# Performance work log

Hardware: AMD Instinct MI355X
Metric: run time of the kernel (lower is better)

The kernel has to match this reference:

```python
import jax, jax.numpy as jnp
import numpy as np

# Gemma2-9B layer config
HID = 3584
H = 16          # query heads
KV = 8          # kv heads
G = H // KV     # GQA group size
DH = 256        # head dim
INTER = 14336
WINDOW = 1024   # sliding window size
LOGIT_CAP = 50.0
SCALING = 256.0 ** -0.5   # query_pre_attn_scalar ** -0.5
EPS = 1e-6
ROPE_BASE = 10000.0
B, S = 2, 2048


def gemma_rmsnorm(x, w, eps=EPS):
    # Gemma RMSNorm: fp32 compute, scale by (1 + w)
    xf = x.astype(jnp.float32)
    var = jnp.mean(xf * xf, axis=-1, keepdims=True)
    return (xf * jax.lax.rsqrt(var + eps) * (1.0 + w.astype(jnp.float32))).astype(x.dtype)


def apply_rope(pos, x):
    # neox-style rotary embedding; x: [B, S, n_heads, DH], pos: [B, S]
    half = DH // 2
    inv_freq = 1.0 / (ROPE_BASE ** (jnp.arange(0, half, dtype=jnp.float32) / half * 1.0))
    inv_freq = 1.0 / (ROPE_BASE ** (jnp.arange(0, DH, 2, dtype=jnp.float32) / DH))
    ang = pos.astype(jnp.float32)[..., None] * inv_freq          # [B, S, half]
    cos = jnp.cos(ang)[:, :, None, :]                            # [B, S, 1, half]
    sin = jnp.sin(ang)[:, :, None, :]
    x1, x2 = x[..., :half], x[..., half:]
    return jnp.concatenate([x1 * cos - x2 * sin, x2 * cos + x1 * sin], axis=-1).astype(x.dtype)


def setup_inputs() -> dict:
    key = jax.random.key(0)
    ks = jax.random.split(key, 12)
    s = 0.02
    inp = {
        "hidden_states": jax.random.normal(ks[0], (B, S, HID), dtype=jnp.float32),
        "positions": jnp.tile(jnp.arange(S, dtype=jnp.int32)[None, :], (B, 1)),
        "in_ln_w": jax.random.normal(ks[1], (HID,), dtype=jnp.float32) * s,
        "post_attn_ln_w": jax.random.normal(ks[2], (HID,), dtype=jnp.float32) * s,
        "pre_ff_ln_w": jax.random.normal(ks[3], (HID,), dtype=jnp.float32) * s,
        "post_ff_ln_w": jax.random.normal(ks[4], (HID,), dtype=jnp.float32) * s,
        "q_w": jax.random.normal(ks[5], (HID, H * DH), dtype=jnp.float32) * s,
        "k_w": jax.random.normal(ks[6], (HID, KV * DH), dtype=jnp.float32) * s,
        "v_w": jax.random.normal(ks[7], (HID, KV * DH), dtype=jnp.float32) * s,
        "o_w": jax.random.normal(ks[8], (H * DH, HID), dtype=jnp.float32) * s,
        "gate_w": jax.random.normal(ks[9], (HID, INTER), dtype=jnp.float32) * s,
        "up_w": jax.random.normal(ks[10], (HID, INTER), dtype=jnp.float32) * s,
        "down_w": jax.random.normal(ks[11], (INTER, HID), dtype=jnp.float32) * s,
    }
    return inp


def _decoder_layer(hidden_states, positions, in_ln_w, post_attn_ln_w, pre_ff_ln_w,
                   post_ff_ln_w, q_w, k_w, v_w, o_w, gate_w, up_w, down_w):
    # residual is None path
    residual = hidden_states
    x = gemma_rmsnorm(hidden_states, in_ln_w)

    # ---- attention ----
    q = (x @ q_w).reshape(B, S, H, DH)
    k = (x @ k_w).reshape(B, S, KV, DH)
    v = (x @ v_w).reshape(B, S, KV, DH)
    q = apply_rope(positions, q)
    k = apply_rope(positions, k)
    kv_fused = jnp.stack([k, v], axis=0)  # paged KV-cache write, modeled densely

    qg = q.reshape(B, S, KV, G, DH)
    # scores: [B, KV, G, S(q), S(k)]
    scores = jnp.einsum('bsngd,btnd->bngst', qg, k) * SCALING
    scores = LOGIT_CAP * jnp.tanh(scores / LOGIT_CAP)  # logit softcapping
    i = jnp.arange(S)[:, None]
    j = jnp.arange(S)[None, :]
    mask = (j <= i) & (i - j < WINDOW)                 # causal + sliding window
    scores = jnp.where(mask, scores, jnp.finfo(scores.dtype).min)
    probs = jax.nn.softmax(scores, axis=-1)
    attn = jnp.einsum('bngst,btnd->bsngd', probs, v).reshape(B, S, H * DH)
    attn_out = attn @ o_w

    x = gemma_rmsnorm(attn_out, post_attn_ln_w)
    x = residual + x
    residual = x

    # ---- GeGLU MLP ----
    x = gemma_rmsnorm(x, pre_ff_ln_w)
    inter = (x @ up_w) * jax.nn.gelu(x @ gate_w)
    x = inter @ down_w
    x = gemma_rmsnorm(x, post_ff_ln_w)
    return x, residual, kv_fused


def reference(hidden_states, positions, in_ln_w, post_attn_ln_w, pre_ff_ln_w,
              post_ff_ln_w, q_w, k_w, v_w, o_w, gate_w, up_w, down_w):
    return _decoder_layer(hidden_states, positions, in_ln_w, post_attn_ln_w,
                          pre_ff_ln_w, post_ff_ln_w, q_w, k_w, v_w, o_w,
                          gate_w, up_w, down_w)
```

## Files before the change

### kernel.cpp

```cpp
#include <hip/hip_runtime.h>
#include <stdint.h>

typedef unsigned short ushortT;
typedef float f32x4 __attribute__((ext_vector_type(4)));
typedef short short8 __attribute__((ext_vector_type(8)));

#define HID 3584
#define NH 16
#define NKV 8
#define DH 256
#define SEQ 2048
#define NB 2
#define NTOK 4096
#define INTERDIM 14336
#define ICH 7168
#define WINDOW 1024

__device__ __forceinline__ ushortT f2bf(float x) {
  union { float f; uint32_t u; } v; v.f = x;
  uint32_t r = v.u + 0x7fffu + ((v.u >> 16) & 1u);
  return (ushortT)(r >> 16);
}
__device__ __forceinline__ float bf2f(uint32_t b) {
  union { uint32_t u; float f; } v; v.u = b << 16;
  return v.f;
}
__device__ __forceinline__ void gll16(const void* g, void* l) {
  __builtin_amdgcn_global_load_lds((const __attribute__((address_space(1))) void*)g,
                                   (__attribute__((address_space(3))) void*)l, 16, 0, 0);
}
__device__ __forceinline__ void sbar() {
  asm volatile("" ::: "memory");
  __builtin_amdgcn_s_barrier();
  asm volatile("" ::: "memory");
}

__global__ __launch_bounds__(256) void transpose_cvt(const float* __restrict__ in,
                                                     ushortT* __restrict__ out,
                                                     int in_rs, int out_rs) {
  __shared__ float tile[64][65];
  const int r0 = blockIdx.y * 64, c0 = blockIdx.x * 64;
  const int t = threadIdx.x, tc = (t & 15) * 4, tr = t >> 4;
#pragma unroll
  for (int p = 0; p < 4; ++p) {
    int r = tr + p * 16;
    float4 v = *(const float4*)&in[(size_t)(r0 + r) * in_rs + c0 + tc];
    tile[r][tc] = v.x; tile[r][tc + 1] = v.y; tile[r][tc + 2] = v.z; tile[r][tc + 3] = v.w;
  }
  __syncthreads();
#pragma unroll
  for (int p = 0; p < 4; ++p) {
    int r = tr + p * 16;
    ushort4 u;
    u.x = f2bf(tile[tc + 0][r]); u.y = f2bf(tile[tc + 1][r]);
    u.z = f2bf(tile[tc + 2][r]); u.w = f2bf(tile[tc + 3][r]);
    *(ushort4*)&out[(size_t)(c0 + r) * out_rs + r0 + tc] = u;
  }
}

__global__ __launch_bounds__(256) void vtrans(const float* __restrict__ vsrc,
                                              ushortT* __restrict__ vT) {
  __shared__ float tile[64][65];
  const int z = blockIdx.z, b = z >> 3, n = z & 7;
  const float* in = vsrc + (size_t)b * SEQ * (NKV * DH) + n * DH;
  ushortT* out = vT + (size_t)z * DH * SEQ;
  const int s0 = blockIdx.y * 64, d0 = blockIdx.x * 64;
  const int t = threadIdx.x, tc = (t & 15) * 4, tr = t >> 4;
#pragma unroll
  for (int p = 0; p < 4; ++p) {
    int r = tr + p * 16;
    float4 v = *(const float4*)&in[(size_t)(s0 + r) * (NKV * DH) + d0 + tc];
    tile[r][tc] = v.x; tile[r][tc + 1] = v.y; tile[r][tc + 2] = v.z; tile[r][tc + 3] = v.w;
  }
  __syncthreads();
#pragma unroll
  for (int p = 0; p < 4; ++p) {
    int r = tr + p * 16;
    ushort4 u;
    u.x = f2bf(tile[tc + 0][r]); u.y = f2bf(tile[tc + 1][r]);
    u.z = f2bf(tile[tc + 2][r]); u.w = f2bf(tile[tc + 3][r]);
    *(ushort4*)&out[(size_t)(d0 + r) * SEQ + s0 + tc] = u;
  }
}

__device__ __forceinline__ float block_sum448(float v, float* sb) {
#pragma unroll
  for (int o = 32; o; o >>= 1) v += __shfl_xor(v, o, 64);
  __syncthreads();
  if ((threadIdx.x & 63) == 0) sb[threadIdx.x >> 6] = v;
  __syncthreads();
  float s = 0.f;
#pragma unroll
  for (int i = 0; i < 7; ++i) s += sb[i];
  return s;
}

__global__ __launch_bounds__(448) void rms_in(const float* __restrict__ in,
                                              const float* __restrict__ w,
                                              ushortT* __restrict__ out) {
  __shared__ float sb[8];
  const size_t row = blockIdx.x;
  const int c = threadIdx.x * 8;
  const float* p = in + row * HID + c;
  float4 a = *(const float4*)p, bq = *(const float4*)(p + 4);
  float v[8] = {a.x, a.y, a.z, a.w, bq.x, bq.y, bq.z, bq.w};
  float ssq = 0.f;
#pragma unroll
  for (int j = 0; j < 8; ++j) ssq += v[j] * v[j];
  float s = block_sum448(ssq, sb);
  float rs = rsqrtf(s * (1.0f / HID) + 1e-6f);
  uint32_t o[4];
#pragma unroll
  for (int j = 0; j < 4; ++j) {
    float r0 = v[2 * j] * rs * (1.f + w[c + 2 * j]);
    float r1 = v[2 * j + 1] * rs * (1.f + w[c + 2 * j + 1]);
    o[j] = (uint32_t)f2bf(r0) | ((uint32_t)f2bf(r1) << 16);
  }
  *(uint4*)(out + row * HID + c) = make_uint4(o[0], o[1], o[2], o[3]);
}

__global__ __launch_bounds__(448) void rms_add(const float* ao,
                                               const float* __restrict__ h,
                                               const float* __restrict__ w1,
                                               const float* __restrict__ w2,
                                               float* resid,
                                               ushortT* __restrict__ x2) {
  __shared__ float sb[8];
  const size_t row = blockIdx.x;
  const int c = threadIdx.x * 8;
  const float* p = ao + row * HID + c;
  float4 a = *(const float4*)p, bq = *(const float4*)(p + 4);
  float v[8] = {a.x, a.y, a.z, a.w, bq.x, bq.y, bq.z, bq.w};
  float ssq = 0.f;
#pragma unroll
  for (int j = 0; j < 8; ++j) ssq += v[j] * v[j];
  float s1 = block_sum448(ssq, sb);
  float rs1 = rsqrtf(s1 * (1.0f / HID) + 1e-6f);
  const float* hp = h + row * HID + c;
  float4 h0 = *(const float4*)hp, h1 = *(const float4*)(hp + 4);
  float hv[8] = {h0.x, h0.y, h0.z, h0.w, h1.x, h1.y, h1.z, h1.w};
  float r[8];
  float ssq2 = 0.f;
#pragma unroll
  for (int j = 0; j < 8; ++j) {
    r[j] = hv[j] + v[j] * rs1 * (1.f + w1[c + j]);
    ssq2 += r[j] * r[j];
  }
  float* rp = resid + row * HID + c;
  *(float4*)rp = make_float4(r[0], r[1], r[2], r[3]);
  *(float4*)(rp + 4) = make_float4(r[4], r[5], r[6], r[7]);
  float s2 = block_sum448(ssq2, sb);
  float rs2 = rsqrtf(s2 * (1.0f / HID) + 1e-6f);
  uint32_t o[4];
#pragma unroll
  for (int j = 0; j < 4; ++j) {
    float q0 = r[2 * j] * rs2 * (1.f + w2[c + 2 * j]);
    float q1 = r[2 * j + 1] * rs2 * (1.f + w2[c + 2 * j + 1]);
    o[j] = (uint32_t)f2bf(q0) | ((uint32_t)f2bf(q1) << 16);
  }
  *(uint4*)(x2 + row * HID + c) = make_uint4(o[0], o[1], o[2], o[3]);
}

__global__ __launch_bounds__(448) void rms_out(const float* in,
                                               const float* __restrict__ w,
                                               float* out) {
  __shared__ float sb[8];
  const size_t row = blockIdx.x;
  const int c = threadIdx.x * 8;
  const float* p = in + row * HID + c;
  float4 a = *(const float4*)p, bq = *(const float4*)(p + 4);
  float v[8] = {a.x, a.y, a.z, a.w, bq.x, bq.y, bq.z, bq.w};
  float ssq = 0.f;
#pragma unroll
  for (int j = 0; j < 8; ++j) ssq += v[j] * v[j];
  float s = block_sum448(ssq, sb);
  float rs = rsqrtf(s * (1.0f / HID) + 1e-6f);
  float* op = out + row * HID + c;
  float r[8];
#pragma unroll
  for (int j = 0; j < 8; ++j) r[j] = v[j] * rs * (1.f + w[c + j]);
  *(float4*)op = make_float4(r[0], r[1], r[2], r[3]);
  *(float4*)(op + 4) = make_float4(r[4], r[5], r[6], r[7]);
}

__global__ __launch_bounds__(128) void rope_q_k(const ushortT* __restrict__ qraw,
                                                const int* __restrict__ pos,
                                                ushortT* __restrict__ qr) {
  const int s = blockIdx.x, h = blockIdx.y, b = blockIdx.z, i = threadIdx.x;
  float p = (float)pos[b * SEQ + s];
  float ang = p * exp2f(-(float)i * (13.287712379549449f / 128.f));
  float sn, cs;
  sincosf(ang, &sn, &cs);
  size_t ib = ((size_t)b * SEQ + s) * (NH * DH) + (size_t)h * DH + i;
  float x1 = bf2f(qraw[ib]), x2 = bf2f(qraw[ib + 128]);
  size_t ob = (((size_t)b * NH + h) * SEQ + s) * DH + i;
  qr[ob] = f2bf(x1 * cs - x2 * sn);
  qr[ob + 128] = f2bf(x2 * cs + x1 * sn);
}

__global__ __launch_bounds__(128) void rope_k_k(const ushortT* __restrict__ kraw,
                                                const int* __restrict__ pos,
                                                ushortT* __restrict__ kr,
                                                float* __restrict__ kv0) {
  const int s = blockIdx.x, n = blockIdx.y, b = blockIdx.z, i = threadIdx.x;
  float p = (float)pos[b * SEQ + s];
  float ang = p * exp2f(-(float)i * (13.287712379549449f / 128.f));
  float sn, cs;
  sincosf(ang, &sn, &cs);
  size_t ib = ((size_t)b * SEQ + s) * (NKV * DH) + (size_t)n * DH + i;
  float x1 = bf2f(kraw[ib]), x2 = bf2f(kraw[ib + 128]);
  float o1 = x1 * cs - x2 * sn, o2 = x2 * cs + x1 * sn;
  size_t ob = (((size_t)b * NKV + n) * SEQ + s) * DH + i;
  kr[ob] = f2bf(o1);
  kr[ob + 128] = f2bf(o2);
  size_t kb = (((size_t)b * SEQ + s) * NKV + n) * DH + i;
  kv0[kb] = o1;
  kv0[kb + 128] = o2;
}

template <int OUTMODE>
__global__ __launch_bounds__(512) void gemm256(const ushortT* __restrict__ A, int lda,
                                               const ushortT* __restrict__ Bt, int ldb,
                                               void* __restrict__ C, int N, int K) {
  __shared__ ushortT lds[73728];
  char* lb = (char*)lds;
  const int tid = threadIdx.x;
  const int nwg = gridDim.x * gridDim.y;
  const int lin = blockIdx.y * gridDim.x + blockIdx.x;
  const int cpx = nwg >> 3;
  const int lin2 = (lin & 7) * cpx + (lin >> 3);
  const int bx = lin2 % gridDim.x, by = lin2 / gridDim.x;
  const int m0 = by * 256, n0 = bx * 128;
  const int l = tid & 63, lr = l & 15, lg = l >> 4;
  const int wid = tid >> 6, wm = wid >> 2, wn = wid & 3;
  const int sr = tid >> 3, sc = tid & 7;

  f32x4 acc[8][2];
#pragma unroll
  for (int i = 0; i < 8; ++i)
#pragma unroll
    for (int j = 0; j < 2; ++j) acc[i][j] = (f32x4){0.f, 0.f, 0.f, 0.f};

  const int nt = K >> 6;
  const ushortT* Ag = A + (size_t)m0 * lda;
  const ushortT* Bg = Bt + (size_t)n0 * ldb;

  auto stageA2 = [&](int tt, int h) {
    char* dst = lb + (tt % 3) * 49152;
    const ushortT* g = Ag + (size_t)tt * 64;
#pragma unroll
    for (int rr = 0; rr < 2; ++rr) {
      int rnd = h * 2 + rr;
      int row = rnd * 64 + sr;
      gll16((const char*)(g + (size_t)row * lda) + ((sc ^ (row & 7)) << 4),
            dst + rnd * 8192 + tid * 16);
    }
  };
  auto stageB1 = [&](int tt, int h) {
    char* dst = lb + (tt % 3) * 49152 + 32768;
    const ushortT* g = Bg + (size_t)tt * 64;
    int row = h * 64 + sr;
    gll16((const char*)(g + (size_t)row * ldb) + ((sc ^ (row & 7)) << 4),
          dst + h * 8192 + tid * 16);
  };

  stageA2(0, 0); stageB1(0, 0); stageA2(0, 1); stageB1(0, 1);
  stageA2(1, 0); stageB1(1, 0); stageA2(1, 1); stageB1(1, 1);
  asm volatile("s_waitcnt vmcnt(6)" ::: "memory");
  sbar();

  for (int t = 0; t < nt; ++t) {
    const char* Ab = lb + (t % 3) * 49152;
    const char* Bb = Ab + 32768;
    short8 af[8], bf[2];
#pragma unroll
    for (int ks = 0; ks < 2; ++ks) {
#pragma unroll
      for (int i = 0; i < 8; ++i) {
        int r = wm * 128 + i * 16 + lr;
        af[i] = *(const short8*)(Ab + r * 128 + (((ks * 4 + lg) ^ (r & 7)) << 4));
      }
#pragma unroll
      for (int j = 0; j < 2; ++j) {
        int r = wn * 32 + j * 16 + lr;
        bf[j] = *(const short8*)(Bb + r * 128 + (((ks * 4 + lg) ^ (r & 7)) << 4));
      }
      if (t + 2 < nt) { stageA2(t + 2, ks); stageB1(t + 2, ks); }
      sbar();
      asm volatile("s_waitcnt lgkmcnt(0)" ::: "memory");
      __builtin_amdgcn_sched_barrier(0);
      __builtin_amdgcn_s_setprio(1);
#pragma unroll
      for (int i = 0; i < 8; ++i)
#pragma unroll
        for (int j = 0; j < 2; ++j)
          acc[i][j] = __builtin_amdgcn_mfma_f32_16x16x32_bf16(af[i], bf[j], acc[i][j], 0, 0, 0);
      __builtin_amdgcn_s_setprio(0);
      if (ks == 1 && t + 1 < nt) {
        if (t + 2 < nt) asm volatile("s_waitcnt vmcnt(6)" ::: "memory");
        else            asm volatile("s_waitcnt vmcnt(0)" ::: "memory");
      }
      sbar();
    }
  }
#pragma unroll
  for (int mi = 0; mi < 8; ++mi)
#pragma unroll
    for (int nj = 0; nj < 2; ++nj)
#pragma unroll
      for (int r = 0; r < 4; ++r) {
        size_t row = (size_t)(m0 + wm * 128 + mi * 16 + lg * 4 + r);
        size_t col = (size_t)(n0 + wn * 32 + nj * 16 + lr);
        if (OUTMODE == 0)
          ((float*)C)[row * N + col] = acc[mi][nj][r];
        else if (OUTMODE == 1)
          ((ushortT*)C)[row * N + col] = f2bf(acc[mi][nj][r]);
        else
          ((float*)C)[row * N + col] += acc[mi][nj][r];
      }
}

__global__ __launch_bounds__(256) void swiglu_k(const ushortT* __restrict__ g,
                                                const ushortT* __restrict__ u,
                                                ushortT* __restrict__ o, int n16) {
  int i = blockIdx.x * 256 + threadIdx.x;
  if (i >= n16) return;
  uint4 gv = ((const uint4*)g)[i];
  uint4 uv = ((const uint4*)u)[i];
  uint32_t ga[4] = {gv.x, gv.y, gv.z, gv.w};
  uint32_t ua[4] = {uv.x, uv.y, uv.z, uv.w};
  uint32_t rr[4];
#pragma unroll
  for (int j = 0; j < 4; ++j) {
    float g0 = bf2f(ga[j] & 0xffffu), g1 = bf2f(ga[j] >> 16);
    float u0 = bf2f(ua[j] & 0xffffu), u1 = bf2f(ua[j] >> 16);
    float e0 = 0.5f * g0 * (1.f + tanhf(0.7978845608f * (g0 + 0.044715f * g0 * g0 * g0)));
    float e1 = 0.5f * g1 * (1.f + tanhf(0.7978845608f * (g1 + 0.044715f * g1 * g1 * g1)));
    rr[j] = (uint32_t)f2bf(u0 * e0) | ((uint32_t)f2bf(u1 * e1) << 16);
  }
  ((uint4*)o)[i] = make_uint4(rr[0], rr[1], rr[2], rr[3]);
}

__global__ __launch_bounds__(256) void attn_fwd(const ushortT* __restrict__ Q,
                                                const ushortT* __restrict__ Kk,
                                                const ushortT* __restrict__ Vt,
                                                ushortT* __restrict__ Out) {
  __shared__ ushortT Kl[32 * 256];
  __shared__ ushortT Vl[256 * 32];
  __shared__ ushortT Pl[4][16 * 32];
  const int tid = threadIdx.x;
  const int w = tid >> 6, l = tid & 63, lr = l & 15, lg = l >> 4;
  const int h = blockIdx.y, b = blockIdx.z;
  const int n = h >> 1;
  const int qs = blockIdx.x * 64;
  const int sw = qs + w * 16;

  const ushortT* qp = Q + (((size_t)b * NH + h) * SEQ + (sw + lr)) * DH;
  short8 qf[8];
#pragma unroll
  for (int kk = 0; kk < 8; ++kk) qf[kk] = *(const short8*)(qp + kk * 32 + lg * 8);

  f32x4 acc[16];
#pragma unroll
  for (int i = 0; i < 16; ++i) acc[i] = (f32x4){0.f, 0.f, 0.f, 0.f};
  float m_s = -1e30f, l_s = 0.f;

  const ushortT* Kbase = Kk + ((size_t)b * NKV + n) * SEQ * DH;
  const ushortT* Vbase = Vt + ((size_t)b * NKV + n) * DH * SEQ;

  int tlo = qs - (WINDOW - 1);
  if (tlo < 0) tlo = 0;
  const int t0b = tlo & ~31;
  const int nt = (qs + 64 - t0b) >> 5;
  const int scol = sw + lr;

  for (int it = 0; it < nt; ++it) {
    const int t0 = t0b + it * 32;
    __syncthreads();
    {
      const int rowk = tid >> 5;
      const int cbk = (tid & 31) * 16;
#pragma unroll
      for (int c = 0; c < 4; ++c) {
        int row = c * 8 + rowk;
        int cbs = cbk ^ ((row & 7) << 4);
        gll16((const char*)(Kbase + (size_t)(t0 + row) * DH) + cbs, (char*)Kl + c * 4096 + tid * 16);
      }
      const int rowv = tid >> 2;
      const int cbv = (tid & 3) * 16;
#pragma unroll
      for (int c = 0; c < 4; ++c) {
        int row = c * 64 + rowv;
        int cbs = cbv ^ ((row & 3) << 4);
        gll16((const char*)(Vbase + (size_t)row * SEQ + t0) + cbs, (char*)Vl + c * 4096 + tid * 16);
      }
    }
    __syncthreads();
    f32x4 st[2];
#pragma unroll
    for (int tt = 0; tt < 2; ++tt) {
      f32x4 a = (f32x4){0.f, 0.f, 0.f, 0.f};
      const int krow = tt * 16 + lr;
      const char* kb = (const char*)Kl + krow * 512;
      const int swz = (krow & 7) << 4;
#pragma unroll
      for (int kk = 0; kk < 8; ++kk) {
        short8 kf = *(const short8*)(kb + ((kk * 64 + lg * 16) ^ swz));
        a = __builtin_amdgcn_mfma_f32_16x16x32_bf16(kf, qf[kk], a, 0, 0, 0);
      }
      st[tt] = a;
    }
    float pvv[8];
    float tmax = -1e30f;
#pragma unroll
    for (int tt = 0; tt < 2; ++tt)
#pragma unroll
      for (int r = 0; r < 4; ++r) {
        int t = t0 + tt * 16 + lg * 4 + r;
        float x = st[tt][r] * 0.0625f;
        x = 50.f * tanhf(x * 0.02f);
        bool ok = (t <= scol) && (scol - t < WINDOW);
        x = ok ? x : -1e30f;
        pvv[tt * 4 + r] = x;
        tmax = fmaxf(tmax, x);
      }
    tmax = fmaxf(tmax, __shfl_xor(tmax, 16, 64));
    tmax = fmaxf(tmax, __shfl_xor(tmax, 32, 64));
    float mnew = fmaxf(m_s, tmax);
    float fsc = __expf(m_s - mnew);
    m_s = mnew;
    float tsum = 0.f;
#pragma unroll
    for (int i = 0; i < 8; ++i) {
      pvv[i] = __expf(pvv[i] - mnew);
      tsum += pvv[i];
    }
    tsum += __shfl_xor(tsum, 16, 64);
    tsum += __shfl_xor(tsum, 32, 64);
    l_s = l_s * fsc + tsum;
    {
      char* pb = (char*)&Pl[w][0] + lr * 64;
      const int pswz = (lr & 3) << 4;
#pragma unroll
      for (int tt = 0; tt < 2; ++tt) {
        uint32_t p01 = (uint32_t)f2bf(pvv[tt * 4 + 0]) | ((uint32_t)f2bf(pvv[tt * 4 + 1]) << 16);
        uint32_t p23 = (uint32_t)f2bf(pvv[tt * 4 + 2]) | ((uint32_t)f2bf(pvv[tt * 4 + 3]) << 16);
        *(uint32_t*)(pb + ((tt * 32 + lg * 8 + 0) ^ pswz)) = p01;
        *(uint32_t*)(pb + ((tt * 32 + lg * 8 + 4) ^ pswz)) = p23;
      }
    }
    float fr[4];
#pragma unroll
    for (int r = 0; r < 4; ++r) fr[r] = __shfl(fsc, lg * 4 + r, 64);
#pragma unroll
    for (int nd = 0; nd < 16; ++nd) {
      acc[nd][0] *= fr[0]; acc[nd][1] *= fr[1];
      acc[nd][2] *= fr[2]; acc[nd][3] *= fr[3];
    }
    const char* pfb = (const char*)&Pl[w][0] + lr * 64;
    short8 pf = *(const short8*)(pfb + ((lg * 16) ^ ((lr & 3) << 4)));
#pragma unroll
    for (int nd = 0; nd < 16; ++nd) {
      const int vrow = nd * 16 + lr;
      short8 vf = *(const short8*)((const char*)Vl + vrow * 64 + ((lg * 16) ^ ((vrow & 3) << 4)));
      acc[nd] = __builtin_amdgcn_mfma_f32_16x16x32_bf16(pf, vf, acc[nd], 0, 0, 0);
    }
  }
  float linv[4];
#pragma unroll
  for (int r = 0; r < 4; ++r) linv[r] = 1.f / __shfl(l_s, lg * 4 + r, 64);
#pragma unroll
  for (int nd = 0; nd < 16; ++nd)
#pragma unroll
    for (int r = 0; r < 4; ++r) {
      size_t row = (size_t)b * SEQ + sw + lg * 4 + r;
      Out[row * (NH * DH) + (size_t)h * DH + nd * 16 + lr] = f2bf(acc[nd][r] * linv[r]);
    }
}

extern "C" void kernel_launch(void* const* d_in, const int* in_sizes, int n_in,
                              void* d_out, int out_size, void* d_ws, size_t ws_size,
                              hipStream_t stream) {
  const float* hs = (const float*)d_in[0];
  const int* pos = (const int*)d_in[1];
  const float* w_in = (const float*)d_in[2];
  const float* w_pa = (const float*)d_in[3];
  const float* w_pf = (const float*)d_in[4];
  const float* w_po = (const float*)d_in[5];
  const float* qw = (const float*)d_in[6];
  const float* kw = (const float*)d_in[7];
  const float* vw = (const float*)d_in[8];
  const float* ow = (const float*)d_in[9];
  const float* gw = (const float*)d_in[10];
  const float* uw = (const float*)d_in[11];
  const float* dw = (const float*)d_in[12];

  float* out_x = (float*)d_out;
  float* out_res = out_x + (size_t)NTOK * HID;
  float* out_kv0 = out_res + (size_t)NTOK * HID;
  float* out_kv1 = out_kv0 + (size_t)NTOK * NKV * DH;

  char* ws = (char*)d_ws;
  char* W = ws;
  ushortT* qwT = (ushortT*)(W);
  ushortT* kwT = (ushortT*)(W + 29360128);
  ushortT* vwT = (ushortT*)(W + 29360128 + 14680064);
  ushortT* owT = (ushortT*)(W + 29360128 + 2 * 14680064);
  ushortT* wS0 = (ushortT*)(W);
  ushortT* wS1 = (ushortT*)(W + 51380224);
  char* R = ws + 102760448;
  ushortT* x1 = (ushortT*)(R);
  ushortT* qraw_b = (ushortT*)(R + 29360128);
  ushortT* kraw_b = (ushortT*)(R + 62914560);
  ushortT* qrope = (ushortT*)(R + 79691776);
  ushortT* krope = (ushortT*)(R + 113246208);
  ushortT* vT = (ushortT*)(R + 130023424);
  ushortT* attnb = qraw_b;
  ushortT* x2 = x1;
  ushortT* gateC = (ushortT*)(R + 29360128);
  ushortT* upC = (ushortT*)(R + 29360128 + 58720256);
  ushortT* interC = gateC;
  float* attn_out = out_res;

  transpose_cvt<<<dim3(4096 / 64, HID / 64), 256, 0, stream>>>(qw, qwT, 4096, HID);
  transpose_cvt<<<dim3(2048 / 64, HID / 64), 256, 0, stream>>>(kw, kwT, 2048, HID);
  transpose_cvt<<<dim3(2048 / 64, HID / 64), 256, 0, stream>>>(vw, vwT, 2048, HID);
  transpose_cvt<<<dim3(HID / 64, 4096 / 64), 256, 0, stream>>>(ow, owT, HID, 4096);

  rms_in<<<NTOK, 448, 0, stream>>>(hs, w_in, x1);

  gemm256<1><<<dim3(32, 16), 512, 0, stream>>>(x1, HID, qwT, HID, qraw_b, 4096, HID);
  gemm256<1><<<dim3(16, 16), 512, 0, stream>>>(x1, HID, kwT, HID, kraw_b, 2048, HID);
  gemm256<0><<<dim3(16, 16), 512, 0, stream>>>(x1, HID, vwT, HID, out_kv1, 2048, HID);

  rope_q_k<<<dim3(SEQ, NH, NB), 128, 0, stream>>>(qraw_b, pos, qrope);
  rope_k_k<<<dim3(SEQ, NKV, NB), 128, 0, stream>>>(kraw_b, pos, krope, out_kv0);
  vtrans<<<dim3(DH / 64, SEQ / 64, NB * NKV), 256, 0, stream>>>(out_kv1, vT);

  attn_fwd<<<dim3(SEQ / 64, NH, NB), 256, 0, stream>>>(qrope, krope, vT, attnb);

  gemm256<0><<<dim3(HID / 128, 16), 512, 0, stream>>>(attnb, 4096, owT, 4096, attn_out, HID, 4096);

  rms_add<<<NTOK, 448, 0, stream>>>(attn_out, hs, w_pa, w_pf, out_res, x2);

  for (int c = 0; c < 2; ++c) {
    transpose_cvt<<<dim3(ICH / 64, HID / 64), 256, 0, stream>>>(gw + (size_t)c * ICH, wS0,
                                                                INTERDIM, HID);
    gemm256<1><<<dim3(ICH / 128, 16), 512, 0, stream>>>(x2, HID, wS0, HID, gateC, ICH, HID);
    transpose_cvt<<<dim3(ICH / 64, HID / 64), 256, 0, stream>>>(uw + (size_t)c * ICH, wS1,
                                                                INTERDIM, HID);
    gemm256<1><<<dim3(ICH / 128, 16), 512, 0, stream>>>(x2, HID, wS1, HID, upC, ICH, HID);
    int n16 = (int)((size_t)NTOK * ICH / 8);
    swiglu_k<<<(n16 + 255) / 256, 256, 0, stream>>>(gateC, upC, interC, n16);
    transpose_cvt<<<dim3(HID / 64, ICH / 64), 256, 0, stream>>>(dw + (size_t)c * ICH * HID, wS0,
                                                                HID, ICH);
    if (c == 0)
      gemm256<0><<<dim3(HID / 128, 16), 512, 0, stream>>>(interC, ICH, wS0, ICH, out_x, HID, ICH);
    else
      gemm256<2><<<dim3(HID / 128, 16), 512, 0, stream>>>(interC, ICH, wS0, ICH, out_x, HID, ICH);
  }

  rms_out<<<NTOK, 448, 0, stream>>>(out_x, w_po, out_x);
}
```

Before: 2.458 ms.

## Switch GEMM to 256x256 tiles with 8-phase double-buffered LDS pipeline

Replaces the 256x128-tile triple-buffered GEMM with a 256x256-tile kernel that double-buffers K-steps in LDS. Each K-step is split into four quarter-tile MFMA phases interleaved with staggered global-to-LDS loads. The larger tile raises arithmetic intensity and halves the number of workgroups. It also doubles the accumulator registers per thread and lengthens the tail on grids that no longer divide evenly (e.g. HID/256=14 columns).

Result: faster. 2.190 ms (-10.9%).

```diff
diff --git a/kernel.cpp b/kernel.cpp
--- a/kernel.cpp
+++ b/kernel.cpp
@@ -219,10 +219,10 @@
 }
 
 template <int OUTMODE>
-__global__ __launch_bounds__(512) void gemm256(const ushortT* __restrict__ A, int lda,
-                                               const ushortT* __restrict__ Bt, int ldb,
-                                               void* __restrict__ C, int N, int K) {
-  __shared__ ushortT lds[73728];
+__global__ __launch_bounds__(512) void gemm8p(const ushortT* __restrict__ A, int lda,
+                                              const ushortT* __restrict__ Bt, int ldb,
+                                              void* __restrict__ C, int N, int K) {
+  __shared__ ushortT lds[65536];
   char* lb = (char*)lds;
   const int tid = threadIdx.x;
   const int nwg = gridDim.x * gridDim.y;
@@ -230,93 +230,129 @@
   const int cpx = nwg >> 3;
   const int lin2 = (lin & 7) * cpx + (lin >> 3);
   const int bx = lin2 % gridDim.x, by = lin2 / gridDim.x;
-  const int m0 = by * 256, n0 = bx * 128;
+  const int m0 = by * 256, n0 = bx * 256;
   const int l = tid & 63, lr = l & 15, lg = l >> 4;
   const int wid = tid >> 6, wm = wid >> 2, wn = wid & 3;
   const int sr = tid >> 3, sc = tid & 7;
 
-  f32x4 acc[8][2];
+  f32x4 acc[8][4];
 #pragma unroll
   for (int i = 0; i < 8; ++i)
 #pragma unroll
-    for (int j = 0; j < 2; ++j) acc[i][j] = (f32x4){0.f, 0.f, 0.f, 0.f};
+    for (int j = 0; j < 4; ++j) acc[i][j] = (f32x4){0.f, 0.f, 0.f, 0.f};
 
   const int nt = K >> 6;
   const ushortT* Ag = A + (size_t)m0 * lda;
   const ushortT* Bg = Bt + (size_t)n0 * ldb;
 
-  auto stageA2 = [&](int tt, int h) {
-    char* dst = lb + (tt % 3) * 49152;
-    const ushortT* g = Ag + (size_t)tt * 64;
-#pragma unroll
-    for (int rr = 0; rr < 2; ++rr) {
-      int rnd = h * 2 + rr;
-      int row = rnd * 64 + sr;
-      gll16((const char*)(g + (size_t)row * lda) + ((sc ^ (row & 7)) << 4),
-            dst + rnd * 8192 + tid * 16);
+  auto stHT = [&](int tt, int op, int h) {
+    char* dst = lb + (tt & 1) * 65536 + op * 32768 + h * 16384;
+    const ushortT* g = (op ? Bg : Ag) + (size_t)tt * 64;
+    const int ld = op ? ldb : lda;
+#pragma unroll
+    for (int L = 0; L < 2; ++L) {
+      int row = h * 128 + L * 64 + sr;
+      gll16((const char*)(g + (size_t)row * ld) + ((sc ^ (row & 7)) << 4),
+            dst + L * 8192 + tid * 16);
     }
   };
-  auto stageB1 = [&](int tt, int h) {
-    char* dst = lb + (tt % 3) * 49152 + 32768;
-    const ushortT* g = Bg + (size_t)tt * 64;
-    int row = h * 64 + sr;
-    gll16((const char*)(g + (size_t)row * ldb) + ((sc ^ (row & 7)) << 4),
-          dst + h * 8192 + tid * 16);
+  short8 afA[4][2], bfA[2][2], bfB[2][2];
+  auto rdA = [&](const char* buf, int mh) {
+#pragma unroll
+    for (int i4 = 0; i4 < 4; ++i4) {
+      int r = wm * 128 + mh * 64 + i4 * 16 + lr;
+      const char* base = buf + wm * 16384 + (r & 127) * 128;
+#pragma unroll
+      for (int ks = 0; ks < 2; ++ks)
+        afA[i4][ks] = *(const short8*)(base + (((ks * 4 + lg) ^ (r & 7)) << 4));
+    }
   };
-
-  stageA2(0, 0); stageB1(0, 0); stageA2(0, 1); stageB1(0, 1);
-  stageA2(1, 0); stageB1(1, 0); stageA2(1, 1); stageB1(1, 1);
-  asm volatile("s_waitcnt vmcnt(6)" ::: "memory");
+  auto rdB = [&](const char* buf, int nh, short8 (*bf)[2]) {
+#pragma unroll
+    for (int j = 0; j < 2; ++j) {
+      int r = wn * 64 + nh * 32 + j * 16 + lr;
+      const char* base = buf + 32768 + (wn >> 1) * 16384 + (r & 127) * 128;
+#pragma unroll
+      for (int ks = 0; ks < 2; ++ks)
+        bf[j][ks] = *(const short8*)(base + (((ks * 4 + lg) ^ (r & 7)) << 4));
+    }
+  };
+  auto mid = [&]() {
+    sbar();
+    asm volatile("s_waitcnt lgkmcnt(0)" ::: "memory");
+    __builtin_amdgcn_sched_barrier(0);
+  };
+  auto mm = [&](int mh, int nh, short8 (*bf)[2]) {
+    __builtin_amdgcn_s_setprio(1);
+#pragma unroll
+    for (int i4 = 0; i4 < 4; ++i4)
+#pragma unroll
+      for (int j = 0; j < 2; ++j)
+#pragma unroll
+        for (int ks = 0; ks < 2; ++ks)
+          acc[mh * 4 + i4][nh * 2 + j] = __builtin_amdgcn_mfma_f32_16x16x32_bf16(
+              afA[i4][ks], bf[j][ks], acc[mh * 4 + i4][nh * 2 + j], 0, 0, 0);
+    __builtin_amdgcn_s_setprio(0);
+  };
+
+  stHT(0, 0, 0); stHT(0, 0, 1); stHT(0, 1, 0); stHT(0, 1, 1);
+  stHT(1, 0, 0); stHT(1, 0, 1); stHT(1, 1, 0); stHT(1, 1, 1);
+  asm volatile("s_waitcnt vmcnt(8)" ::: "memory");
   sbar();
 
-  for (int t = 0; t < nt; ++t) {
-    const char* Ab = lb + (t % 3) * 49152;
-    const char* Bb = Ab + 32768;
-    short8 af[8], bf[2];
-#pragma unroll
-    for (int ks = 0; ks < 2; ++ks) {
-#pragma unroll
-      for (int i = 0; i < 8; ++i) {
-        int r = wm * 128 + i * 16 + lr;
-        af[i] = *(const short8*)(Ab + r * 128 + (((ks * 4 + lg) ^ (r & 7)) << 4));
-      }
-#pragma unroll
-      for (int j = 0; j < 2; ++j) {
-        int r = wn * 32 + j * 16 + lr;
-        bf[j] = *(const short8*)(Bb + r * 128 + (((ks * 4 + lg) ^ (r & 7)) << 4));
-      }
-      if (t + 2 < nt) { stageA2(t + 2, ks); stageB1(t + 2, ks); }
-      sbar();
-      asm volatile("s_waitcnt lgkmcnt(0)" ::: "memory");
-      __builtin_amdgcn_sched_barrier(0);
-      __builtin_amdgcn_s_setprio(1);
-#pragma unroll
-      for (int i = 0; i < 8; ++i)
-#pragma unroll
-        for (int j = 0; j < 2; ++j)
-          acc[i][j] = __builtin_amdgcn_mfma_f32_16x16x32_bf16(af[i], bf[j], acc[i][j], 0, 0, 0);
-      __builtin_amdgcn_s_setprio(0);
-      if (ks == 1 && t + 1 < nt) {
-        if (t + 2 < nt) asm volatile("s_waitcnt vmcnt(6)" ::: "memory");
-        else            asm volatile("s_waitcnt vmcnt(0)" ::: "memory");
-      }
-      sbar();
-    }
+  const int nit = nt >> 1;
+  const char* b0 = lb;
+  const char* b1 = lb + 65536;
+  for (int i = 0; i < nit; ++i) {
+    const int t1 = 2 * i + 1, s0 = 2 * i + 2, s1 = 2 * i + 3;
+    const bool hs0 = s0 < nt, hs1 = s1 < nt, pre = i > 0;
+    rdA(b0, 0);
+    rdB(b0, 0, bfA);
+    if (pre) stHT(t1, 0, 1);
+    asm volatile("s_waitcnt lgkmcnt(8)" ::: "memory");
+    mid(); mm(0, 0, bfA); sbar();
+    rdB(b0, 1, bfB);
+    if (pre) stHT(t1, 1, 1);
+    mid(); mm(0, 1, bfB); sbar();
+    rdA(b0, 1);
+    if (hs0) stHT(s0, 1, 0);
+    mid(); mm(1, 0, bfA); sbar();
+    if (hs0) stHT(s0, 0, 0);
+    mid(); mm(1, 1, bfB);
+    if (hs0) asm volatile("s_waitcnt vmcnt(4)" ::: "memory");
+    else     asm volatile("s_waitcnt vmcnt(0)" ::: "memory");
+    sbar();
+    rdA(b1, 0);
+    rdB(b1, 0, bfA);
+    if (hs0) stHT(s0, 0, 1);
+    asm volatile("s_waitcnt lgkmcnt(8)" ::: "memory");
+    mid(); mm(0, 0, bfA); sbar();
+    rdB(b1, 1, bfB);
+    if (hs0) stHT(s0, 1, 1);
+    mid(); mm(0, 1, bfB); sbar();
+    rdA(b1, 1);
+    if (hs1) stHT(s1, 1, 0);
+    mid(); mm(1, 0, bfA); sbar();
+    if (hs1) stHT(s1, 0, 0);
+    mid(); mm(1, 1, bfB);
+    if (hs1) asm volatile("s_waitcnt vmcnt(4)" ::: "memory");
+    sbar();
   }
 #pragma unroll
   for (int mi = 0; mi < 8; ++mi)
 #pragma unroll
-    for (int nj = 0; nj < 2; ++nj)
+    for (int nj = 0; nj < 4; ++nj)
 #pragma unroll
       for (int r = 0; r < 4; ++r) {
         size_t row = (size_t)(m0 + wm * 128 + mi * 16 + lg * 4 + r);
-        size_t col = (size_t)(n0 + wn * 32 + nj * 16 + lr);
+        size_t col = (size_t)(n0 + wn * 64 + nj * 16 + lr);
+        size_t idx = row * N + col;
         if (OUTMODE == 0)
-          ((float*)C)[row * N + col] = acc[mi][nj][r];
+          ((float*)C)[idx] = acc[mi][nj][r];
         else if (OUTMODE == 1)
-          ((ushortT*)C)[row * N + col] = f2bf(acc[mi][nj][r]);
+          ((ushortT*)C)[idx] = f2bf(acc[mi][nj][r]);
         else
-          ((float*)C)[row * N + col] += acc[mi][nj][r];
+          ((float*)C)[idx] += acc[mi][nj][r];
       }
 }
 
@@ -529,9 +565,9 @@
 
   rms_in<<<NTOK, 448, 0, stream>>>(hs, w_in, x1);
 
-  gemm256<1><<<dim3(32, 16), 512, 0, stream>>>(x1, HID, qwT, HID, qraw_b, 4096, HID);
-  gemm256<1><<<dim3(16, 16), 512, 0, stream>>>(x1, HID, kwT, HID, kraw_b, 2048, HID);
-  gemm256<0><<<dim3(16, 16), 512, 0, stream>>>(x1, HID, vwT, HID, out_kv1, 2048, HID);
+  gemm8p<1><<<dim3(16, 16), 512, 0, stream>>>(x1, HID, qwT, HID, qraw_b, 4096, HID);
+  gemm8p<1><<<dim3(8, 16), 512, 0, stream>>>(x1, HID, kwT, HID, kraw_b, 2048, HID);
+  gemm8p<0><<<dim3(8, 16), 512, 0, stream>>>(x1, HID, vwT, HID, out_kv1, 2048, HID);
 
   rope_q_k<<<dim3(SEQ, NH, NB), 128, 0, stream>>>(qraw_b, pos, qrope);
   rope_k_k<<<dim3(SEQ, NKV, NB), 128, 0, stream>>>(kraw_b, pos, krope, out_kv0);
@@ -539,25 +575,25 @@
 
   attn_fwd<<<dim3(SEQ / 64, NH, NB), 256, 0, stream>>>(qrope, krope, vT, attnb);
 
-  gemm256<0><<<dim3(HID / 128, 16), 512, 0, stream>>>(attnb, 4096, owT, 4096, attn_out, HID, 4096);
+  gemm8p<0><<<dim3(HID / 256, 16), 512, 0, stream>>>(attnb, 4096, owT, 4096, attn_out, HID, 4096);
 
   rms_add<<<NTOK, 448, 0, stream>>>(attn_out, hs, w_pa, w_pf, out_res, x2);
 
   for (int c = 0; c < 2; ++c) {
     transpose_cvt<<<dim3(ICH / 64, HID / 64), 256, 0, stream>>>(gw + (size_t)c * ICH, wS0,
                                                                 INTERDIM, HID);
-    gemm256<1><<<dim3(ICH / 128, 16), 512, 0, stream>>>(x2, HID, wS0, HID, gateC, ICH, HID);
+    gemm8p<1><<<dim3(ICH / 256, 16), 512, 0, stream>>>(x2, HID, wS0, HID, gateC, ICH, HID);
     transpose_cvt<<<dim3(ICH / 64, HID / 64), 256, 0, stream>>>(uw + (size_t)c * ICH, wS1,
                                                                 INTERDIM, HID);
-    gemm256<1><<<dim3(ICH / 128, 16), 512, 0, stream>>>(x2, HID, wS1, HID, upC, ICH, HID);
+    gemm8p<1><<<dim3(ICH / 256, 16), 512, 0, stream>>>(x2, HID, wS1, HID, upC, ICH, HID);
     int n16 = (int)((size_t)NTOK * ICH / 8);
     swiglu_k<<<(n16 + 255) / 256, 256, 0, stream>>>(gateC, upC, interC, n16);
     transpose_cvt<<<dim3(HID / 64, ICH / 64), 256, 0, stream>>>(dw + (size_t)c * ICH * HID, wS0,
                                                                 HID, ICH);
     if (c == 0)
-      gemm256<0><<<dim3(HID / 128, 16), 512, 0, stream>>>(interC, ICH, wS0, ICH, out_x, HID, ICH);
+      gemm8p<0><<<dim3(HID / 256, 16), 512, 0, stream>>>(interC, ICH, wS0, ICH, out_x, HID, ICH);
     else
-      gemm256<2><<<dim3(HID / 128, 16), 512, 0, stream>>>(interC, ICH, wS0, ICH, out_x, HID, ICH);
+      gemm8p<2><<<dim3(HID / 256, 16), 512, 0, stream>>>(interC, ICH, wS0, ICH, out_x, HID, ICH);
   }
 
   rms_out<<<NTOK, 448, 0, stream>>>(out_x, w_po, out_x);
```
